# Kernel tuning notes

Hardware: AMD Instinct MI355X
Metric: run time of the kernel (lower is better)

## Reference

```python
import jax, jax.numpy as jnp
import numpy as np

IN_FEATURES = 1024
OUT_FEATURES = 1280
K = 16  # intermediate_features
B_EXTRA = OUT_FEATURES - IN_FEATURES  # 256
N = 256


def setup_inputs() -> dict:
    key = jax.random.key(0)
    k1, k2 = jax.random.split(key)
    x = jax.random.normal(k1, (N, IN_FEATURES), dtype=jnp.float32)
    T = jax.random.normal(k2, (IN_FEATURES, B_EXTRA, K), dtype=jnp.float32) * 0.02
    return {"x": x, "T": T}


def reference(x, T):
    # M: (N, B_extra, K)
    M = jnp.einsum('ni,ibk->nbk', x, T)
    # pairwise L1 over K: (N, N, B_extra)
    l1 = jnp.abs(M[:, None, :, :] - M[None, :, :, :]).sum(axis=3)
    # sum over the other-sample axis, subtract self term exp(0)=1
    out = jnp.exp(-l1).sum(axis=0) - 1.0  # (N, B_extra)
    return jnp.concatenate([x, out], axis=1)  # (N, OUT_FEATURES)
```

## Files before the change

kernel.cpp:

```cpp
#include <hip/hip_runtime.h>
#include <hip/hip_fp16.h>
#include <hip/hip_bf16.h>

#define NB 256
#define IN_F 1024
#define BEX 256
#define KD 16
#define NJ 4096
#define OUT_F 1280

typedef short bf16x8 __attribute__((ext_vector_type(8)));
typedef float f32x4 __attribute__((ext_vector_type(4)));
typedef _Float16 h2 __attribute__((ext_vector_type(2)));

__device__ inline unsigned short f2bf(float f) {
    __hip_bfloat16 h = __float2bfloat16(f);
    return *reinterpret_cast<unsigned short*>(&h);
}

__device__ inline void cp16(const void* g, void* l) {
    __builtin_amdgcn_global_load_lds((const __attribute__((address_space(1))) void*)g,
                                     (__attribute__((address_space(3))) void*)l, 16, 0, 0);
}

union U8 { float4 f4[2]; h2 h[8]; };

__global__ __launch_bounds__(256) void k_prep(const float* __restrict__ x,
                                              const float* __restrict__ T,
                                              float* __restrict__ out,
                                              unsigned short* __restrict__ x_bf,
                                              unsigned short* __restrict__ Tt) {
    const int bid = blockIdx.x;
    const int t = threadIdx.x;
    if (bid < 4096) {
        __shared__ float tile[32][33];
        const int j0 = (bid & 127) * 32;
        const int i0 = (bid >> 7) * 32;
        {
            const int r = t >> 3, cg = (t & 7) << 2;
            float4 v = *(const float4*)(T + (size_t)(i0 + r) * NJ + j0 + cg);
            tile[r][cg + 0] = v.x; tile[r][cg + 1] = v.y;
            tile[r][cg + 2] = v.z; tile[r][cg + 3] = v.w;
        }
        __syncthreads();
        const int jr = t >> 3, ig = (t & 7) << 2;
        ushort4 o;
        o.x = f2bf(tile[ig + 0][jr]);
        o.y = f2bf(tile[ig + 1][jr]);
        o.z = f2bf(tile[ig + 2][jr]);
        o.w = f2bf(tile[ig + 3][jr]);
        *(ushort4*)(Tt + (size_t)(j0 + jr) * IN_F + i0 + ig) = o;
    } else {
        const int r = bid - 4096;
        float4 v = *(const float4*)(x + (size_t)r * IN_F + t * 4);
        *(float4*)(out + (size_t)r * OUT_F + t * 4) = v;
        ushort4 o;
        o.x = f2bf(v.x); o.y = f2bf(v.y); o.z = f2bf(v.z); o.w = f2bf(v.w);
        *(ushort4*)(x_bf + (size_t)r * IN_F + t * 4) = o;
    }
}

__global__ __launch_bounds__(256) void k_gemm(const unsigned short* __restrict__ A,
                                              const unsigned short* __restrict__ B,
                                              __half* __restrict__ M2h) {
    __shared__ unsigned short lds[4][64 * 128];
    const int t = threadIdx.x;
    const int w = t >> 6, l = t & 63;
    const int n0 = blockIdx.y * 64;
    const int j0 = blockIdx.x * 64;

    const unsigned short* aA[4];
    const unsigned short* aB[4];
    int lofs[4];
    #pragma unroll
    for (int p = 0; p < 4; ++p) {
        int s = t + p * 256;
        int r = s >> 4;
        int kg = (s & 15) ^ (r & 15);
        aA[p] = A + (size_t)(n0 + r) * IN_F + kg * 8;
        aB[p] = B + (size_t)(j0 + r) * IN_F + kg * 8;
        lofs[p] = s * 8;
    }

    f32x4 acc[2][2];
    #pragma unroll
    for (int i = 0; i < 2; ++i)
        #pragma unroll
        for (int j = 0; j < 2; ++j)
            acc[i][j] = (f32x4){0.f, 0.f, 0.f, 0.f};

    #pragma unroll
    for (int p = 0; p < 4; ++p) cp16(aA[p], &lds[0][lofs[p]]);
    #pragma unroll
    for (int p = 0; p < 4; ++p) cp16(aB[p], &lds[1][lofs[p]]);

    const int rowA0 = ((w & 1) * 32 + (l & 15)) * 128;
    const int rowA1 = rowA0 + 16 * 128;
    const int rowB0 = (((w >> 1) & 1) * 32 + (l & 15)) * 128;
    const int rowB1 = rowB0 + 16 * 128;

    for (int s = 0; s < 8; ++s) {
        __syncthreads();
        if (s < 7) {
            const int k0 = (s + 1) * 128;
            const int bsel = ((s + 1) & 1) * 2;
            #pragma unroll
            for (int p = 0; p < 4; ++p) cp16(aA[p] + k0, &lds[bsel + 0][lofs[p]]);
            #pragma unroll
            for (int p = 0; p < 4; ++p) cp16(aB[p] + k0, &lds[bsel + 1][lofs[p]]);
        }
        const unsigned short* La = lds[(s & 1) * 2 + 0];
        const unsigned short* Lb = lds[(s & 1) * 2 + 1];
        #pragma unroll
        for (int kk = 0; kk < 4; ++kk) {
            const int kg = kk * 4 + (l >> 4);
            const int ks = (kg ^ (l & 15)) * 8;
            bf16x8 a0 = *(const bf16x8*)&La[rowA0 + ks];
            bf16x8 a1 = *(const bf16x8*)&La[rowA1 + ks];
            bf16x8 b0 = *(const bf16x8*)&Lb[rowB0 + ks];
            bf16x8 b1 = *(const bf16x8*)&Lb[rowB1 + ks];
            acc[0][0] = __builtin_amdgcn_mfma_f32_16x16x32_bf16(a0, b0, acc[0][0], 0, 0, 0);
            acc[0][1] = __builtin_amdgcn_mfma_f32_16x16x32_bf16(a0, b1, acc[0][1], 0, 0, 0);
            acc[1][0] = __builtin_amdgcn_mfma_f32_16x16x32_bf16(a1, b0, acc[1][0], 0, 0, 0);
            acc[1][1] = __builtin_amdgcn_mfma_f32_16x16x32_bf16(a1, b1, acc[1][1], 0, 0, 0);
        }
    }

    const int col = l & 15;
    #pragma unroll
    for (int nt = 0; nt < 2; ++nt) {
        #pragma unroll
        for (int jt = 0; jt < 2; ++jt) {
            const int jc = j0 + ((w >> 1) & 1) * 32 + jt * 16 + col;
            const int bb = jc >> 4;
            const int k = jc & 15;
            __half* base = M2h + (size_t)bb * (NB * KD) + k;
            #pragma unroll
            for (int r = 0; r < 4; ++r) {
                const int n = n0 + (w & 1) * 32 + nt * 16 + (l >> 4) * 4 + r;
                base[n * KD] = __float2half(acc[nt][jt][r]);
            }
        }
    }
}

__global__ __launch_bounds__(512) void k_pairwise(const __half* __restrict__ M2h,
                                                  float* __restrict__ out) {
    __shared__ __half rows[NB * KD];
    __shared__ float Sm[NB];
    __shared__ float part[NB * 8];
    const int b = blockIdx.x;
    const int t = threadIdx.x;
    const int lane = t & 63, w = t >> 6;
    const int qq = t & 15;
    const int mm = t >> 4;
    const __half* Mb = M2h + (size_t)b * (NB * KD);

    {
        float4 v = ((const float4*)Mb)[t];
        ((float4*)rows)[t ^ ((t >> 3) & 7)] = v;
    }
    if (t < NB) Sm[t] = 0.f;
    __syncthreads();

    const h2 one = {(_Float16)1.0f, (_Float16)1.0f};

    #pragma unroll
    for (int ti = 0; ti < 4; ++ti) {
        U8 q[4];
        #pragma unroll
        for (int r = 0; r < 4; ++r) {
            const int n = ti * 64 + qq * 4 + r;
            const int sw = (n >> 2) & 7;
            q[r].f4[0] = ((const float4*)rows)[(n * 2) ^ sw];
            q[r].f4[1] = ((const float4*)rows)[(n * 2 + 1) ^ sw];
        }
        float eq[4] = {0.f, 0.f, 0.f, 0.f};

        for (int tj = ti; tj < 4; ++tj) {
            const int m0 = tj * 64 + mm * 2;
            const int sw = (m0 >> 2) & 7;
            U8 p0, p1;
            p0.f4[0] = ((const float4*)rows)[(m0 * 2) ^ sw];
            p0.f4[1] = ((const float4*)rows)[(m0 * 2 + 1) ^ sw];
            p1.f4[0] = ((const float4*)rows)[(m0 * 2 + 2) ^ sw];
            p1.f4[1] = ((const float4*)rows)[(m0 * 2 + 3) ^ sw];

            float pm0 = 0.f, pm1 = 0.f;
            #pragma unroll
            for (int r = 0; r < 4; ++r) {
                float a0 = 0.f, a1 = 0.f, b0 = 0.f, b1 = 0.f;
                #pragma unroll
                for (int i = 0; i < 8; i += 2) {
                    h2 d0 = q[r].h[i] - p0.h[i];
                    h2 d1 = q[r].h[i + 1] - p0.h[i + 1];
                    h2 d2 = q[r].h[i] - p1.h[i];
                    h2 d3 = q[r].h[i + 1] - p1.h[i + 1];
                    unsigned u0 = (*(unsigned*)&d0) & 0x7FFF7FFFu;
                    unsigned u1 = (*(unsigned*)&d1) & 0x7FFF7FFFu;
                    unsigned u2 = (*(unsigned*)&d2) & 0x7FFF7FFFu;
                    unsigned u3 = (*(unsigned*)&d3) & 0x7FFF7FFFu;
                    a0 = __builtin_amdgcn_fdot2(*(h2*)&u0, one, a0, false);
                    a1 = __builtin_amdgcn_fdot2(*(h2*)&u1, one, a1, false);
                    b0 = __builtin_amdgcn_fdot2(*(h2*)&u2, one, b0, false);
                    b1 = __builtin_amdgcn_fdot2(*(h2*)&u3, one, b1, false);
                }
                const float e0 = __expf(-(a0 + a1));
                const float e1 = __expf(-(b0 + b1));
                eq[r] += e0 + e1;
                pm0 += e0;
                pm1 += e1;
            }
            if (tj > ti) {
                #pragma unroll
                for (int s = 1; s < 16; s <<= 1) {
                    pm0 += __shfl_xor(pm0, s);
                    pm1 += __shfl_xor(pm1, s);
                }
                if (qq == 0) {
                    Sm[m0] += pm0;
                    Sm[m0 + 1] += pm1;
                }
            }
        }
        #pragma unroll
        for (int r = 0; r < 4; ++r) {
            eq[r] += __shfl_xor(eq[r], 16);
            eq[r] += __shfl_xor(eq[r], 32);
        }
        if (lane < 16) {
            #pragma unroll
            for (int r = 0; r < 4; ++r)
                part[(ti * 64 + lane * 4 + r) * 8 + w] = eq[r];
        }
    }
    __syncthreads();

    if (t < NB) {
        const float* pp = &part[t * 8];
        float s = Sm[t] - 1.f;
        #pragma unroll
        for (int i = 0; i < 8; ++i) s += pp[i];
        out[(size_t)t * OUT_F + IN_F + b] = s;
    }
}

extern "C" void kernel_launch(void* const* d_in, const int* in_sizes, int n_in,
                              void* d_out, int out_size, void* d_ws, size_t ws_size,
                              hipStream_t stream) {
    const float* x = (const float*)d_in[0];
    const float* T = (const float*)d_in[1];
    float* out = (float*)d_out;

    char* ws = (char*)d_ws;
    unsigned short* x_bf = (unsigned short*)ws;
    unsigned short* Tt   = (unsigned short*)(ws + (1u << 19));
    __half* M2h          = (__half*)(ws + (1u << 19) + (1u << 23));

    k_prep<<<dim3(4352), dim3(256), 0, stream>>>(x, T, out, x_bf, Tt);
    k_gemm<<<dim3(64, 4), dim3(256), 0, stream>>>(x_bf, Tt, M2h);
    k_pairwise<<<dim3(256), dim3(512), 0, stream>>>(M2h, out);
}
```

Baseline: 91.49 us.

## Split pairwise triangle work across two blocks per feature with atomic accumulation

The pairwise kernel now launches two blocks per extra feature, each taking half of the upper-triangular 64x64 tile pairs (5 tiles each). Partial sums are combined with atomicAdd into the output, which the prep kernel pre-initialises to -1 to account for the self term. The aim is to double the block count from 256 to 512 so more of the GPU's compute units are busy. The cost is float atomics with nondeterministic summation order and a duplicated LDS load of the feature rows in each block.

```diff
diff --git a/kernel.cpp b/kernel.cpp
--- a/kernel.cpp
+++ b/kernel.cpp
@@ -57,6 +57,9 @@
         ushort4 o;
         o.x = f2bf(v.x); o.y = f2bf(v.y); o.z = f2bf(v.z); o.w = f2bf(v.w);
         *(ushort4*)(x_bf + (size_t)r * IN_F + t * 4) = o;
+        if (t < 64)
+            *(float4*)(out + (size_t)r * OUT_F + IN_F + t * 4) =
+                make_float4(-1.f, -1.f, -1.f, -1.f);
     }
 }
 
@@ -150,79 +153,81 @@
     __shared__ float Sm[NB];
     __shared__ float part[NB * 8];
     const int b = blockIdx.x;
+    const int y = blockIdx.y;
     const int t = threadIdx.x;
     const int lane = t & 63, w = t >> 6;
     const int qq = t & 15;
     const int mm = t >> 4;
     const __half* Mb = M2h + (size_t)b * (NB * KD);
 
-    {
-        float4 v = ((const float4*)Mb)[t];
-        ((float4*)rows)[t ^ ((t >> 3) & 7)] = v;
-    }
+    ((float4*)rows)[t ^ ((t >> 3) & 7)] = ((const float4*)Mb)[t];
     if (t < NB) Sm[t] = 0.f;
+    ((float4*)part)[t] = make_float4(0.f, 0.f, 0.f, 0.f);
     __syncthreads();
 
     const h2 one = {(_Float16)1.0f, (_Float16)1.0f};
-
-    #pragma unroll
-    for (int ti = 0; ti < 4; ++ti) {
-        U8 q[4];
+    U8 q[4];
+    float eq[4];
+
+    auto load_q = [&](int ti) {
         #pragma unroll
         for (int r = 0; r < 4; ++r) {
             const int n = ti * 64 + qq * 4 + r;
             const int sw = (n >> 2) & 7;
             q[r].f4[0] = ((const float4*)rows)[(n * 2) ^ sw];
             q[r].f4[1] = ((const float4*)rows)[(n * 2 + 1) ^ sw];
-        }
-        float eq[4] = {0.f, 0.f, 0.f, 0.f};
-
-        for (int tj = ti; tj < 4; ++tj) {
-            const int m0 = tj * 64 + mm * 2;
-            const int sw = (m0 >> 2) & 7;
-            U8 p0, p1;
-            p0.f4[0] = ((const float4*)rows)[(m0 * 2) ^ sw];
-            p0.f4[1] = ((const float4*)rows)[(m0 * 2 + 1) ^ sw];
-            p1.f4[0] = ((const float4*)rows)[(m0 * 2 + 2) ^ sw];
-            p1.f4[1] = ((const float4*)rows)[(m0 * 2 + 3) ^ sw];
-
-            float pm0 = 0.f, pm1 = 0.f;
-            #pragma unroll
-            for (int r = 0; r < 4; ++r) {
-                float a0 = 0.f, a1 = 0.f, b0 = 0.f, b1 = 0.f;
-                #pragma unroll
-                for (int i = 0; i < 8; i += 2) {
-                    h2 d0 = q[r].h[i] - p0.h[i];
-                    h2 d1 = q[r].h[i + 1] - p0.h[i + 1];
-                    h2 d2 = q[r].h[i] - p1.h[i];
-                    h2 d3 = q[r].h[i + 1] - p1.h[i + 1];
-                    unsigned u0 = (*(unsigned*)&d0) & 0x7FFF7FFFu;
-                    unsigned u1 = (*(unsigned*)&d1) & 0x7FFF7FFFu;
-                    unsigned u2 = (*(unsigned*)&d2) & 0x7FFF7FFFu;
-                    unsigned u3 = (*(unsigned*)&d3) & 0x7FFF7FFFu;
-                    a0 = __builtin_amdgcn_fdot2(*(h2*)&u0, one, a0, false);
-                    a1 = __builtin_amdgcn_fdot2(*(h2*)&u1, one, a1, false);
-                    b0 = __builtin_amdgcn_fdot2(*(h2*)&u2, one, b0, false);
-                    b1 = __builtin_amdgcn_fdot2(*(h2*)&u3, one, b1, false);
-                }
-                const float e0 = __expf(-(a0 + a1));
-                const float e1 = __expf(-(b0 + b1));
-                eq[r] += e0 + e1;
-                pm0 += e0;
-                pm1 += e1;
-            }
-            if (tj > ti) {
-                #pragma unroll
-                for (int s = 1; s < 16; s <<= 1) {
-                    pm0 += __shfl_xor(pm0, s);
-                    pm1 += __shfl_xor(pm1, s);
-                }
-                if (qq == 0) {
-                    Sm[m0] += pm0;
-                    Sm[m0 + 1] += pm1;
-                }
-            }
-        }
+            eq[r] = 0.f;
+        }
+    };
+
+    auto do_tile = [&](int ti, int tj) {
+        const int m0 = tj * 64 + mm * 2;
+        const int sw = (m0 >> 2) & 7;
+        U8 p0, p1;
+        p0.f4[0] = ((const float4*)rows)[(m0 * 2) ^ sw];
+        p0.f4[1] = ((const float4*)rows)[(m0 * 2 + 1) ^ sw];
+        p1.f4[0] = ((const float4*)rows)[(m0 * 2 + 2) ^ sw];
+        p1.f4[1] = ((const float4*)rows)[(m0 * 2 + 3) ^ sw];
+
+        float pm0 = 0.f, pm1 = 0.f;
+        #pragma unroll
+        for (int r = 0; r < 4; ++r) {
+            float a0 = 0.f, a1 = 0.f, b0 = 0.f, b1 = 0.f;
+            #pragma unroll
+            for (int i = 0; i < 8; i += 2) {
+                h2 d0 = q[r].h[i] - p0.h[i];
+                h2 d1 = q[r].h[i + 1] - p0.h[i + 1];
+                h2 d2 = q[r].h[i] - p1.h[i];
+                h2 d3 = q[r].h[i + 1] - p1.h[i + 1];
+                unsigned u0 = (*(unsigned*)&d0) & 0x7FFF7FFFu;
+                unsigned u1 = (*(unsigned*)&d1) & 0x7FFF7FFFu;
+                unsigned u2 = (*(unsigned*)&d2) & 0x7FFF7FFFu;
+                unsigned u3 = (*(unsigned*)&d3) & 0x7FFF7FFFu;
+                a0 = __builtin_amdgcn_fdot2(*(h2*)&u0, one, a0, false);
+                a1 = __builtin_amdgcn_fdot2(*(h2*)&u1, one, a1, false);
+                b0 = __builtin_amdgcn_fdot2(*(h2*)&u2, one, b0, false);
+                b1 = __builtin_amdgcn_fdot2(*(h2*)&u3, one, b1, false);
+            }
+            const float e0 = __expf(-(a0 + a1));
+            const float e1 = __expf(-(b0 + b1));
+            eq[r] += e0 + e1;
+            pm0 += e0;
+            pm1 += e1;
+        }
+        if (tj != ti) {
+            #pragma unroll
+            for (int s = 1; s < 16; s <<= 1) {
+                pm0 += __shfl_xor(pm0, s);
+                pm1 += __shfl_xor(pm1, s);
+            }
+            if (qq == 0) {
+                Sm[m0] += pm0;
+                Sm[m0 + 1] += pm1;
+            }
+        }
+    };
+
+    auto flush_q = [&](int ti) {
         #pragma unroll
         for (int r = 0; r < 4; ++r) {
             eq[r] += __shfl_xor(eq[r], 16);
@@ -233,15 +238,24 @@
             for (int r = 0; r < 4; ++r)
                 part[(ti * 64 + lane * 4 + r) * 8 + w] = eq[r];
         }
+    };
+
+    if (y == 0) {
+        load_q(0); do_tile(0, 0); do_tile(0, 1); do_tile(0, 2); do_tile(0, 3); flush_q(0);
+        load_q(1); do_tile(1, 1); flush_q(1);
+    } else {
+        load_q(1); do_tile(1, 2); do_tile(1, 3); flush_q(1);
+        load_q(2); do_tile(2, 2); do_tile(2, 3); flush_q(2);
+        load_q(3); do_tile(3, 3); flush_q(3);
     }
     __syncthreads();
 
     if (t < NB) {
         const float* pp = &part[t * 8];
-        float s = Sm[t] - 1.f;
+        float s = Sm[t];
         #pragma unroll
         for (int i = 0; i < 8; ++i) s += pp[i];
-        out[(size_t)t * OUT_F + IN_F + b] = s;
+        atomicAdd(&out[(size_t)t * OUT_F + IN_F + b], s);
     }
 }
 
@@ -259,5 +273,5 @@
 
     k_prep<<<dim3(4352), dim3(256), 0, stream>>>(x, T, out, x_bf, Tt);
     k_gemm<<<dim3(64, 4), dim3(256), 0, stream>>>(x_bf, Tt, M2h);
-    k_pairwise<<<dim3(256), dim3(512), 0, stream>>>(M2h, out);
-}
+    k_pairwise<<<dim3(256, 2), dim3(512), 0, stream>>>(M2h, out);
+}
```

After: 92.01 us. About the same (+0.6%).
